# Optimization experiments

Hardware: AMD Instinct MI355X
Metric: run time of the kernel (lower is better)

Reference implementation:

```python
import jax, jax.numpy as jnp
import numpy as np

B, DIN, HID, DOUT, E, TOPK = 8192, 1024, 2048, 1024, 8, 2
GHID = HID // 2  # gating hidden


def setup_inputs() -> dict:
    key = jax.random.key(0)
    ks = jax.random.split(key, 16)
    s = lambda fan_in: 1.0 / np.sqrt(fan_in)
    return {
        "x": jax.random.normal(ks[0], (B, DIN), dtype=jnp.float32),
        # stacked expert params, leading axis = expert
        "w1": jax.random.uniform(ks[1], (E, DIN, HID), jnp.float32, -s(DIN), s(DIN)),
        "b1": jax.random.uniform(ks[2], (E, HID), jnp.float32, -s(DIN), s(DIN)),
        "w2": jax.random.uniform(ks[3], (E, HID, HID), jnp.float32, -s(HID), s(HID)),
        "b2": jax.random.uniform(ks[4], (E, HID), jnp.float32, -s(HID), s(HID)),
        "w3": jax.random.uniform(ks[5], (E, HID, DOUT), jnp.float32, -s(HID), s(HID)),
        "b3": jax.random.uniform(ks[6], (E, DOUT), jnp.float32, -s(HID), s(HID)),
        "wp": jax.random.uniform(ks[7], (E, DIN, HID), jnp.float32, -s(DIN), s(DIN)),
        "bp": jax.random.uniform(ks[8], (E, HID), jnp.float32, -s(DIN), s(DIN)),
        # gating network: Linear(DIN, GHID) -> ReLU -> Linear(GHID, E)
        "gw1": jax.random.uniform(ks[9], (DIN, GHID), jnp.float32, -s(DIN), s(DIN)),
        "gb1": jax.random.uniform(ks[10], (GHID,), jnp.float32, -s(DIN), s(DIN)),
        "gw2": jax.random.uniform(ks[11], (GHID, E), jnp.float32, -s(GHID), s(GHID)),
        "gb2": jax.random.uniform(ks[12], (E,), jnp.float32, -s(GHID), s(GHID)),
    }


def reference(x, w1, b1, w2, b2, w3, b3, wp, bp, gw1, gb1, gw2, gb2):
    # gating: [B, E]
    gate_logits = jnp.maximum(x @ gw1 + gb1, 0.0) @ gw2 + gb2
    topk_w, topk_i = jax.lax.top_k(gate_logits, TOPK)  # [B, K]
    topk_w = jax.nn.softmax(topk_w, axis=1)
    # dense per-expert residual MLP (dropout is identity in eval mode)
    h = jnp.maximum(jnp.einsum('bi,eih->beh', x, w1) + b1, 0.0)  # [B,E,HID]
    out = jnp.einsum('beh,ehg->beg', h, w2) + b2                  # [B,E,HID]
    identity = jnp.einsum('bi,eih->beh', x, wp) + bp              # projection
    out = jnp.maximum(out + identity, 0.0)
    expert_out = jnp.einsum('beh,eho->beo', out, w3) + b3         # [B,E,DOUT]
    # scatter top-k weights into dense [B, E] gate
    gate = jnp.zeros_like(gate_logits).at[jnp.arange(x.shape[0])[:, None], topk_i].set(topk_w)
    return jnp.einsum('beo,be->bo', expert_out, gate)             # [B, DOUT]
```

## Files before the change

### kernel.cpp

```cpp
#include <hip/hip_runtime.h>
#include <hip/hip_bf16.h>
#include <cstdint>
#include <cstddef>

#define TOK  8192
#define DIN  1024
#define HID  2048
#define DOUTN 1024
#define NEXP 8
#define GHID 1024

typedef __attribute__((ext_vector_type(8))) short bf16x8;
typedef __attribute__((ext_vector_type(4))) float floatx4;

__device__ __forceinline__ unsigned short f2b(float f) {
  unsigned int u = __float_as_uint(f);
  u += 0x7fffu + ((u >> 16) & 1u);
  return (unsigned short)(u >> 16);
}

__device__ __forceinline__ float b2f(unsigned short b) {
  return __uint_as_float(((unsigned int)b) << 16);
}

__device__ __forceinline__ void async_cp16(const unsigned short* g, char* lds) {
  __builtin_amdgcn_global_load_lds(
      (const __attribute__((address_space(1))) unsigned int*)g,
      (__attribute__((address_space(3))) unsigned int*)lds, 16, 0, 0);
}


__global__ void cvt_x_kernel(const float* __restrict__ src,
                             unsigned short* __restrict__ xb,
                             unsigned short* __restrict__ xcat, int n4) {
  int i = blockIdx.x * blockDim.x + threadIdx.x;
  if (i >= n4) return;
  float4 v = ((const float4*)src)[i];
  ushort4 hi, lo;
  hi.x = f2b(v.x); lo.x = f2b(v.x - b2f(hi.x));
  hi.y = f2b(v.y); lo.y = f2b(v.y - b2f(hi.y));
  hi.z = f2b(v.z); lo.z = f2b(v.z - b2f(hi.z));
  hi.w = f2b(v.w); lo.w = f2b(v.w - b2f(hi.w));
  ((ushort4*)xb)[i] = hi;
  int t = i >> 8;
  int kk = i & 255;
  ushort4* rowc = (ushort4*)(xcat + (size_t)t * 3072);
  rowc[kk] = hi;
  rowc[256 + kk] = hi;
  rowc[512 + kk] = lo;
}

__global__ void cvt_transpose_kernel(const float* __restrict__ src,
                                     unsigned short* __restrict__ dst,
                                     int K, int N) {
  __shared__ float tile[32][33];
  long e = blockIdx.z;
  src += e * (long)K * N;
  dst += e * (long)K * N;
  int n0 = blockIdx.x * 32, k0 = blockIdx.y * 32;
  int x = threadIdx.x, y = threadIdx.y;
#pragma unroll
  for (int i = 0; i < 4; i++)
    tile[y + 8 * i][x] = src[(long)(k0 + y + 8 * i) * N + n0 + x];
  __syncthreads();
#pragma unroll
  for (int i = 0; i < 4; i++)
    dst[(long)(n0 + y + 8 * i) * K + k0 + x] = f2b(tile[x][y + 8 * i]);
}

__global__ void cvt_gw1_kernel(const float* __restrict__ src,
                               unsigned short* __restrict__ dst) {
  __shared__ float tile[32][33];
  int n0 = blockIdx.x * 32, k0 = blockIdx.y * 32;
  int x = threadIdx.x, y = threadIdx.y;
#pragma unroll
  for (int i = 0; i < 4; i++)
    tile[y + 8 * i][x] = src[(long)(k0 + y + 8 * i) * GHID + n0 + x];
  __syncthreads();
#pragma unroll
  for (int i = 0; i < 4; i++) {
    float v = tile[x][y + 8 * i];
    unsigned short hi = f2b(v);
    unsigned short lo = f2b(v - b2f(hi));
    size_t r = (size_t)(n0 + y + 8 * i) * 3072 + k0 + x;
    dst[r] = hi;
    dst[r + 1024] = lo;
    dst[r + 2048] = hi;
  }
}


#define KLOOP(pa0, pa1, pb0, pb1, NKT)                                        \
  for (int kt = 0; kt < (NKT); ++kt) {                                        \
    __syncthreads();                                                          \
    async_cp16((pa0) + kt * 32, ldsA0);                                       \
    async_cp16((pa1) + kt * 32, ldsA0 + 4096);                                \
    async_cp16((pb0) + kt * 32, ldsB0);                                       \
    async_cp16((pb1) + kt * 32, ldsB0 + 4096);                                \
    __syncthreads();                                                          \
    bf16x8 af[4], bfr[4];                                                     \
    _Pragma("unroll") for (int i = 0; i < 4; i++) {                           \
      af[i] = *(const bf16x8*)(AsB + i * 1024);                               \
      bfr[i] = *(const bf16x8*)(BsB + i * 1024);                              \
    }                                                                         \
    _Pragma("unroll") for (int mi = 0; mi < 4; mi++)                          \
      _Pragma("unroll") for (int ni = 0; ni < 4; ni++)                        \
        acc[mi][ni] = __builtin_amdgcn_mfma_f32_16x16x32_bf16(                \
            af[mi], bfr[ni], acc[mi][ni], 0, 0, 0);                           \
  }

#define TILE_SETUP()                                                          \
  int tid = threadIdx.x;                                                      \
  int sr = tid >> 2;                                                          \
  int lchunk = (tid & 3) ^ ((sr >> 1) & 3);                                   \
  int koffA = lchunk * 8;                                                     \
  char* ldsA0 = (char*)As + (tid & 192) * 16;                                 \
  char* ldsB0 = (char*)Bs + (tid & 192) * 16;                                 \
  int lane = tid & 63, wv = tid >> 6;                                         \
  int wm = (wv >> 1) << 6, wn = (wv & 1) << 6;                                \
  int q = lane >> 4, l15 = lane & 15;                                         \
  int abase = l15 * 64 + ((q ^ ((l15 >> 1) & 3)) << 4);                       \
  const char* AsB = (const char*)As + wm * 64 + abase;                        \
  const char* BsB = (const char*)Bs + wn * 64 + abase;                        \
  floatx4 acc[4][4] = {};


__global__ __launch_bounds__(256, 2) void gating_mfma(
    const unsigned short* __restrict__ xcat,
    const unsigned short* __restrict__ gw1t3,
    const float* __restrict__ gb1, float* __restrict__ H) {
  __shared__ __align__(16) unsigned short As[128 * 32];
  __shared__ __align__(16) unsigned short Bs[128 * 32];
  TILE_SETUP();
  int row0 = blockIdx.y << 7, tn = blockIdx.x << 7;

  const unsigned short* a0p = xcat + (size_t)(row0 + sr) * 3072 + koffA;
  const unsigned short* a1p = xcat + (size_t)(row0 + 64 + sr) * 3072 + koffA;
  const unsigned short* b0p = gw1t3 + (size_t)(tn + sr) * 3072 + koffA;
  const unsigned short* b1p = gw1t3 + (size_t)(tn + 64 + sr) * 3072 + koffA;

  KLOOP(a0p, a1p, b0p, b1p, 3072 / 32);

  int crow = row0 + wm + q * 4;
  int ccol0 = tn + wn + l15;
#pragma unroll
  for (int ni = 0; ni < 4; ++ni) {
    int col = ccol0 + ni * 16;
    float bias = gb1[col];
#pragma unroll
    for (int mi = 0; mi < 4; ++mi)
#pragma unroll
      for (int rg = 0; rg < 4; ++rg) {
        int rr = crow + mi * 16 + rg;
        H[(size_t)rr * GHID + col] = fmaxf(acc[mi][ni][rg] + bias, 0.f);
      }
  }
}


__global__ void gating2_topk(const float* __restrict__ H,
                             const float* __restrict__ gw2,
                             const float* __restrict__ gb2,
                             int* __restrict__ gidx, float* __restrict__ gwt) {
  int wv = threadIdx.x >> 6, lane = threadIdx.x & 63;
  int t = blockIdx.x * 4 + wv;
  const float* hrow = H + (size_t)t * GHID;
  float acc[8] = {};
  for (int k = lane; k < GHID; k += 64) {
    float v = hrow[k];
    float4 g0 = *(const float4*)(gw2 + (size_t)k * 8);
    float4 g1 = *(const float4*)(gw2 + (size_t)k * 8 + 4);
    acc[0] += v * g0.x; acc[1] += v * g0.y; acc[2] += v * g0.z; acc[3] += v * g0.w;
    acc[4] += v * g1.x; acc[5] += v * g1.y; acc[6] += v * g1.z; acc[7] += v * g1.w;
  }
#pragma unroll
  for (int off = 32; off > 0; off >>= 1)
#pragma unroll
    for (int e = 0; e < 8; e++) acc[e] += __shfl_xor(acc[e], off);

  if (lane == 0) {
    float l[8];
#pragma unroll
    for (int e = 0; e < 8; e++) l[e] = acc[e] + gb2[e];
    int b0 = 0; float v0 = l[0];
#pragma unroll
    for (int e = 1; e < 8; e++) if (l[e] > v0) { v0 = l[e]; b0 = e; }
    int b1 = -1; float v1 = -3.4e38f;
#pragma unroll
    for (int e = 0; e < 8; e++)
      if (e != b0 && l[e] > v1) { v1 = l[e]; b1 = e; }
    float ex = expf(v1 - v0);
    float inv = 1.f / (1.f + ex);
    gidx[2 * t] = b0; gidx[2 * t + 1] = b1;
    gwt[2 * t] = inv; gwt[2 * t + 1] = ex * inv;
  }
}


__global__ void route_count(const int* __restrict__ gidx, int* cnt) {
  int t = blockIdx.x * blockDim.x + threadIdx.x;
  int lane = threadIdx.x & 63;
  int e0 = gidx[2 * t], e1 = gidx[2 * t + 1];
#pragma unroll 1
  for (int e = 0; e < NEXP; e++) {
    unsigned long long m0 = __ballot(e0 == e);
    if (m0 && lane == __ffsll(m0) - 1) atomicAdd(&cnt[e], (int)__popcll(m0));
    unsigned long long m1 = __ballot(e1 == e);
    if (m1 && lane == __ffsll(m1) - 1) atomicAdd(&cnt[e], (int)__popcll(m1));
  }
}

__global__ void route_scan(const int* __restrict__ cnt, int* base_, int* cur) {
  if (threadIdx.x == 0) {
    int s = 0;
    for (int e = 0; e < NEXP; e++) { base_[e] = s; cur[e] = s; s += cnt[e]; }
  }
}

__global__ void route_scatter(const int* __restrict__ gidx,
                              const float* __restrict__ gwt, int* cur,
                              int* __restrict__ rt, float* __restrict__ rw) {
  int t = blockIdx.x * blockDim.x + threadIdx.x;
  int lane = threadIdx.x & 63;
  int e0 = gidx[2 * t], e1 = gidx[2 * t + 1];
  float w0 = gwt[2 * t], w1 = gwt[2 * t + 1];
#pragma unroll 1
  for (int e = 0; e < NEXP; e++) {
#pragma unroll 1
    for (int s = 0; s < 2; s++) {
      int mye = s ? e1 : e0;
      unsigned long long m = __ballot(mye == e);
      if (m) {
        int leader = __ffsll(m) - 1;
        int bb = 0;
        if (lane == leader) bb = atomicAdd(&cur[e], (int)__popcll(m));
        bb = __shfl(bb, leader);
        if (mye == e) {
          int pos = bb + (int)__popcll(m & ((1ull << lane) - 1ull));
          rt[pos] = t;
          rw[pos] = s ? w1 : w0;
        }
      }
    }
  }
}


template <int MODE>
__global__ __launch_bounds__(256, 2) void moe_gemm(
    const unsigned short* __restrict__ xb, const unsigned short* __restrict__ hbuf,
    const unsigned short* __restrict__ obuf, const unsigned short* __restrict__ w1t,
    const unsigned short* __restrict__ wpt, const unsigned short* __restrict__ w2t,
    const unsigned short* __restrict__ w3t, const float* __restrict__ b1,
    const float* __restrict__ b2, const float* __restrict__ bp,
    const float* __restrict__ b3, const int* __restrict__ rt,
    const float* __restrict__ rw, const int* __restrict__ cnt,
    const int* __restrict__ base, unsigned short* __restrict__ hout,
    unsigned short* __restrict__ oout, float* __restrict__ dout) {
  __shared__ __align__(16) unsigned short As[128 * 32];
  __shared__ __align__(16) unsigned short Bs[128 * 32];

  int lt = blockIdx.y;
  int e = 0, cn = 0, ok = 0;
  for (e = 0; e < NEXP; ++e) {
    int c = cnt[e];
    int nt = (c + 127) >> 7;
    if (lt < nt) { cn = c; ok = 1; break; }
    lt -= nt;
  }
  if (!ok) return;
  int be = base[e];
  int row0 = lt << 7;
  int tn = blockIdx.x << 7;

  TILE_SETUP();

  int rl0 = row0 + sr, rl1 = row0 + 64 + sr;
  int cl0 = min(rl0, cn - 1), cl1 = min(rl1, cn - 1);

  if (MODE == 1) {
    const unsigned short* a0p = xb + (size_t)rt[be + cl0] * DIN + koffA;
    const unsigned short* a1p = xb + (size_t)rt[be + cl1] * DIN + koffA;
    const unsigned short* bw0 = w1t + ((size_t)e * HID + tn + sr) * DIN + koffA;
    const unsigned short* bw1 = w1t + ((size_t)e * HID + tn + 64 + sr) * DIN + koffA;
    KLOOP(a0p, a1p, bw0, bw1, DIN / 32);
  } else if (MODE == 2) {
    const unsigned short* a0p = hbuf + (size_t)(be + cl0) * HID + koffA;
    const unsigned short* a1p = hbuf + (size_t)(be + cl1) * HID + koffA;
    const unsigned short* bw0 = w2t + (size_t)e * HID * HID + (size_t)(tn + sr) * HID + koffA;
    const unsigned short* bw1 = w2t + (size_t)e * HID * HID + (size_t)(tn + 64 + sr) * HID + koffA;
    KLOOP(a0p, a1p, bw0, bw1, HID / 32);
    const unsigned short* a0q = xb + (size_t)rt[be + cl0] * DIN + koffA;
    const unsigned short* a1q = xb + (size_t)rt[be + cl1] * DIN + koffA;
    const unsigned short* bq0 = wpt + (size_t)e * HID * DIN + (size_t)(tn + sr) * DIN + koffA;
    const unsigned short* bq1 = wpt + (size_t)e * HID * DIN + (size_t)(tn + 64 + sr) * DIN + koffA;
    KLOOP(a0q, a1q, bq0, bq1, DIN / 32);
  } else {
    const unsigned short* a0p = obuf + (size_t)(be + cl0) * HID + koffA;
    const unsigned short* a1p = obuf + (size_t)(be + cl1) * HID + koffA;
    const unsigned short* bw0 = w3t + (size_t)e * DOUTN * HID + (size_t)(tn + sr) * HID + koffA;
    const unsigned short* bw1 = w3t + (size_t)e * DOUTN * HID + (size_t)(tn + 64 + sr) * HID + koffA;
    KLOOP(a0p, a1p, bw0, bw1, HID / 32);
  }

  int crow = row0 + wm + q * 4;
  int ccol0 = tn + wn + l15;
  if (MODE == 1) {
    const float* bb = b1 + (size_t)e * HID;
#pragma unroll
    for (int ni = 0; ni < 4; ++ni) {
      int col = ccol0 + ni * 16;
      float bias = bb[col];
#pragma unroll
      for (int mi = 0; mi < 4; ++mi)
#pragma unroll
        for (int rg = 0; rg < 4; ++rg) {
          int rr = crow + mi * 16 + rg;
          if (rr < cn) {
            float v = fmaxf(acc[mi][ni][rg] + bias, 0.f);
            hout[(size_t)(be + rr) * HID + col] = f2b(v);
          }
        }
    }
  } else if (MODE == 2) {
    const float* bb = b2 + (size_t)e * HID;
    const float* bq = bp + (size_t)e * HID;
#pragma unroll
    for (int ni = 0; ni < 4; ++ni) {
      int col = ccol0 + ni * 16;
      float bias = bb[col] + bq[col];
#pragma unroll
      for (int mi = 0; mi < 4; ++mi)
#pragma unroll
        for (int rg = 0; rg < 4; ++rg) {
          int rr = crow + mi * 16 + rg;
          if (rr < cn) {
            float v = fmaxf(acc[mi][ni][rg] + bias, 0.f);
            oout[(size_t)(be + rr) * HID + col] = f2b(v);
          }
        }
    }
  } else {
    const float* bb = b3 + (size_t)e * DOUTN;
    float biasv[4];
#pragma unroll
    for (int ni = 0; ni < 4; ++ni) biasv[ni] = bb[ccol0 + ni * 16];
#pragma unroll
    for (int mi = 0; mi < 4; ++mi)
#pragma unroll
      for (int rg = 0; rg < 4; ++rg) {
        int rr = crow + mi * 16 + rg;
        if (rr < cn) {
          int tk = rt[be + rr];
          float wgt = rw[be + rr];
#pragma unroll
          for (int ni = 0; ni < 4; ++ni) {
            int col = ccol0 + ni * 16;
            atomicAdd(dout + (size_t)tk * DOUTN + col,
                      (acc[mi][ni][rg] + biasv[ni]) * wgt);
          }
        }
      }
  }
}


extern "C" void kernel_launch(void* const* d_in, const int* in_sizes, int n_in,
                              void* d_out, int out_size, void* d_ws,
                              size_t ws_size, hipStream_t stream) {
  const float* x = (const float*)d_in[0];
  const float* w1 = (const float*)d_in[1];
  const float* b1 = (const float*)d_in[2];
  const float* w2 = (const float*)d_in[3];
  const float* b2 = (const float*)d_in[4];
  const float* w3 = (const float*)d_in[5];
  const float* b3 = (const float*)d_in[6];
  const float* wp = (const float*)d_in[7];
  const float* bp = (const float*)d_in[8];
  const float* gw1 = (const float*)d_in[9];
  const float* gb1 = (const float*)d_in[10];
  const float* gw2 = (const float*)d_in[11];
  const float* gb2 = (const float*)d_in[12];
  float* outp = (float*)d_out;
  char* ws = (char*)d_ws;

  const size_t o_w1t = 0;
  const size_t o_wpt = o_w1t + (size_t)NEXP * HID * DIN * 2;
  const size_t o_w2t = o_wpt + (size_t)NEXP * HID * DIN * 2;
  const size_t o_w3t = o_w2t + (size_t)NEXP * HID * HID * 2;
  const size_t o_xb  = o_w3t + (size_t)NEXP * DOUTN * HID * 2;
  const size_t o_hg  = o_xb + (size_t)TOK * DIN * 2;
  const size_t o_h   = o_hg + (size_t)TOK * GHID * 4;
  const size_t o_ob  = o_h + (size_t)2 * TOK * HID * 2;
  const size_t o_gidx = o_ob + (size_t)2 * TOK * HID * 2;
  const size_t o_gw  = o_gidx + (size_t)2 * TOK * 4;
  const size_t o_cnt = o_gw + (size_t)2 * TOK * 4;
  const size_t o_base = o_cnt + 128;
  const size_t o_cur = o_base + 128;
  const size_t o_rt  = o_cur + 128;
  const size_t o_rw  = o_rt + (size_t)2 * TOK * 4;
  const size_t o_xcat = o_ob;
  const size_t o_gw1t3 = o_h;

  unsigned short* w1t = (unsigned short*)(ws + o_w1t);
  unsigned short* wpt = (unsigned short*)(ws + o_wpt);
  unsigned short* w2t = (unsigned short*)(ws + o_w2t);
  unsigned short* w3t = (unsigned short*)(ws + o_w3t);
  unsigned short* xb = (unsigned short*)(ws + o_xb);
  float* hg = (float*)(ws + o_hg);
  unsigned short* hbuf = (unsigned short*)(ws + o_h);
  unsigned short* obuf = (unsigned short*)(ws + o_ob);
  unsigned short* xcat = (unsigned short*)(ws + o_xcat);
  unsigned short* gw1t3 = (unsigned short*)(ws + o_gw1t3);
  int* gidx = (int*)(ws + o_gidx);
  float* gwt = (float*)(ws + o_gw);
  int* cnt = (int*)(ws + o_cnt);
  int* basep = (int*)(ws + o_base);
  int* cur = (int*)(ws + o_cur);
  int* rtl = (int*)(ws + o_rt);
  float* rwl = (float*)(ws + o_rw);

  hipMemsetAsync(d_out, 0, (size_t)out_size * 4, stream);
  hipMemsetAsync(ws + o_cnt, 0, 32, stream);

  cvt_x_kernel<<<dim3(TOK * DIN / 4 / 256), 256, 0, stream>>>(x, xb, xcat, TOK * DIN / 4);
  cvt_gw1_kernel<<<dim3(GHID / 32, DIN / 32), dim3(32, 8), 0, stream>>>(gw1, gw1t3);
  cvt_transpose_kernel<<<dim3(HID / 32, DIN / 32, NEXP), dim3(32, 8), 0, stream>>>(w1, w1t, DIN, HID);
  cvt_transpose_kernel<<<dim3(HID / 32, DIN / 32, NEXP), dim3(32, 8), 0, stream>>>(wp, wpt, DIN, HID);
  cvt_transpose_kernel<<<dim3(HID / 32, HID / 32, NEXP), dim3(32, 8), 0, stream>>>(w2, w2t, HID, HID);
  cvt_transpose_kernel<<<dim3(DOUTN / 32, HID / 32, NEXP), dim3(32, 8), 0, stream>>>(w3, w3t, HID, DOUTN);

  gating_mfma<<<dim3(GHID / 128, TOK / 128), 256, 0, stream>>>(xcat, gw1t3, gb1, hg);
  gating2_topk<<<dim3(TOK / 4), 256, 0, stream>>>(hg, gw2, gb2, gidx, gwt);
  route_count<<<dim3(TOK / 256), 256, 0, stream>>>(gidx, cnt);
  route_scan<<<1, 64, 0, stream>>>(cnt, basep, cur);
  route_scatter<<<dim3(TOK / 256), 256, 0, stream>>>(gidx, gwt, cur, rtl, rwl);

  moe_gemm<1><<<dim3(HID / 128, 135), 256, 0, stream>>>(
      xb, hbuf, obuf, w1t, wpt, w2t, w3t, b1, b2, bp, b3, rtl, rwl, cnt, basep,
      hbuf, obuf, outp);
  moe_gemm<2><<<dim3(HID / 128, 135), 256, 0, stream>>>(
      xb, hbuf, obuf, w1t, wpt, w2t, w3t, b1, b2, bp, b3, rtl, rwl, cnt, basep,
      hbuf, obuf, outp);
  moe_gemm<3><<<dim3(DOUTN / 128, 135), 256, 0, stream>>>(
      xb, hbuf, obuf, w1t, wpt, w2t, w3t, b1, b2, bp, b3, rtl, rwl, cnt, basep,
      hbuf, obuf, outp);
}
```

Baseline: 1.123 ms.

## Concatenate h and gathered x into one K=3072 operand, replace atomics with combine

Rows are pre-gathered into a contiguous hx buffer ([h | x] per routed slot), and w2 and wp are packed into one [HID, 3072] weight, so MODE 2 runs a single K-loop instead of two with indirect x loads. The final GEMM writes weighted per-slot outputs to a scratch buffer, and a combine kernel sums each token's two slots, replacing atomicAdd and the output memset. Weight transposes use a wider 64x64 tile with vectorized stores, and launch bounds rise to 4 blocks per SM. The cost is extra gather and combine kernels plus more workspace, and the higher occupancy target may cause register spills.

Result: no change. 1.118 ms (-0.5%).

```diff
diff --git a/kernel.cpp b/kernel.cpp
--- a/kernel.cpp
+++ b/kernel.cpp
@@ -12,6 +12,7 @@
 
 typedef __attribute__((ext_vector_type(8))) short bf16x8;
 typedef __attribute__((ext_vector_type(4))) float floatx4;
+typedef __attribute__((ext_vector_type(8))) unsigned short ushort8v;
 
 __device__ __forceinline__ unsigned short f2b(float f) {
   unsigned int u = __float_as_uint(f);
@@ -50,22 +51,35 @@
   rowc[512 + kk] = lo;
 }
 
-__global__ void cvt_transpose_kernel(const float* __restrict__ src,
-                                     unsigned short* __restrict__ dst,
-                                     int K, int N) {
-  __shared__ float tile[32][33];
+__global__ void cvt_transpose_v2(const float* __restrict__ src,
+                                 unsigned short* __restrict__ dst, int N,
+                                 long sEstride, long dEstride, int ldDst) {
+  __shared__ __align__(16) unsigned short t[64][72];
   long e = blockIdx.z;
-  src += e * (long)K * N;
-  dst += e * (long)K * N;
-  int n0 = blockIdx.x * 32, k0 = blockIdx.y * 32;
-  int x = threadIdx.x, y = threadIdx.y;
-#pragma unroll
-  for (int i = 0; i < 4; i++)
-    tile[y + 8 * i][x] = src[(long)(k0 + y + 8 * i) * N + n0 + x];
+  src += e * sEstride;
+  dst += e * dEstride;
+  int n0 = blockIdx.x * 64, k0 = blockIdx.y * 64;
+  int tid = threadIdx.x;
+  int kr = tid >> 2, qc = tid & 3;
+  const float* s = src + (long)(k0 + kr) * N + n0 + qc * 16;
+#pragma unroll
+  for (int i = 0; i < 4; i++) {
+    float4 v = *(const float4*)(s + i * 4);
+    int nn = qc * 16 + i * 4;
+    t[nn + 0][kr] = f2b(v.x);
+    t[nn + 1][kr] = f2b(v.y);
+    t[nn + 2][kr] = f2b(v.z);
+    t[nn + 3][kr] = f2b(v.w);
+  }
   __syncthreads();
-#pragma unroll
-  for (int i = 0; i < 4; i++)
-    dst[(long)(n0 + y + 8 * i) * K + k0 + x] = f2b(tile[x][y + 8 * i]);
+  int c = tid & 7;
+  int nr = tid >> 3;
+#pragma unroll
+  for (int p = 0; p < 2; p++) {
+    int n = nr + 32 * p;
+    ushort8v v = *(const ushort8v*)&t[n][c * 8];
+    *(ushort8v*)(dst + (long)(n0 + n) * ldDst + k0 + c * 8) = v;
+  }
 }
 
 __global__ void cvt_gw1_kernel(const float* __restrict__ src,
@@ -125,7 +139,7 @@
   floatx4 acc[4][4] = {};
 
 
-__global__ __launch_bounds__(256, 2) void gating_mfma(
+__global__ __launch_bounds__(256, 4) void gating_mfma(
     const unsigned short* __restrict__ xcat,
     const unsigned short* __restrict__ gw1t3,
     const float* __restrict__ gb1, float* __restrict__ H) {
@@ -219,7 +233,8 @@
 
 __global__ void route_scatter(const int* __restrict__ gidx,
                               const float* __restrict__ gwt, int* cur,
-                              int* __restrict__ rt, float* __restrict__ rw) {
+                              int* __restrict__ rt, float* __restrict__ rw,
+                              int* __restrict__ inv) {
   int t = blockIdx.x * blockDim.x + threadIdx.x;
   int lane = threadIdx.x & 63;
   int e0 = gidx[2 * t], e1 = gidx[2 * t + 1];
@@ -239,24 +254,46 @@
           int pos = bb + (int)__popcll(m & ((1ull << lane) - 1ull));
           rt[pos] = t;
           rw[pos] = s ? w1 : w0;
+          inv[2 * t + s] = pos;
         }
       }
     }
   }
 }
 
+__global__ void xgather_kernel(const unsigned short* __restrict__ xb,
+                               const int* __restrict__ rt,
+                               unsigned short* __restrict__ hx) {
+  int slot = blockIdx.x;
+  int c = threadIdx.x;
+  int t = rt[slot];
+  ((ushort8v*)(hx + (size_t)slot * 3072 + 2048))[c] =
+      ((const ushort8v*)(xb + (size_t)t * 1024))[c];
+}
+
+__global__ void combine_kernel(const float* __restrict__ s3,
+                               const int* __restrict__ inv,
+                               float* __restrict__ out) {
+  int t = blockIdx.x;
+  int c = threadIdx.x;
+  const float4* r0 = (const float4*)(s3 + (size_t)inv[2 * t] * DOUTN);
+  const float4* r1 = (const float4*)(s3 + (size_t)inv[2 * t + 1] * DOUTN);
+  float4 a = r0[c], b = r1[c];
+  float4 o = {a.x + b.x, a.y + b.y, a.z + b.z, a.w + b.w};
+  ((float4*)(out + (size_t)t * DOUTN))[c] = o;
+}
+
 
 template <int MODE>
-__global__ __launch_bounds__(256, 2) void moe_gemm(
-    const unsigned short* __restrict__ xb, const unsigned short* __restrict__ hbuf,
-    const unsigned short* __restrict__ obuf, const unsigned short* __restrict__ w1t,
-    const unsigned short* __restrict__ wpt, const unsigned short* __restrict__ w2t,
+__global__ __launch_bounds__(256, 4) void moe_gemm(
+    const unsigned short* __restrict__ hx, const unsigned short* __restrict__ obuf,
+    const unsigned short* __restrict__ w1t, const unsigned short* __restrict__ w2p,
     const unsigned short* __restrict__ w3t, const float* __restrict__ b1,
     const float* __restrict__ b2, const float* __restrict__ bp,
-    const float* __restrict__ b3, const int* __restrict__ rt,
-    const float* __restrict__ rw, const int* __restrict__ cnt,
-    const int* __restrict__ base, unsigned short* __restrict__ hout,
-    unsigned short* __restrict__ oout, float* __restrict__ dout) {
+    const float* __restrict__ b3, const float* __restrict__ rw,
+    const int* __restrict__ cnt, const int* __restrict__ base,
+    unsigned short* __restrict__ hxout, unsigned short* __restrict__ oout,
+    float* __restrict__ s3) {
   __shared__ __align__(16) unsigned short As[128 * 32];
   __shared__ __align__(16) unsigned short Bs[128 * 32];
 
@@ -279,27 +316,22 @@
   int cl0 = min(rl0, cn - 1), cl1 = min(rl1, cn - 1);
 
   if (MODE == 1) {
-    const unsigned short* a0p = xb + (size_t)rt[be + cl0] * DIN + koffA;
-    const unsigned short* a1p = xb + (size_t)rt[be + cl1] * DIN + koffA;
+    const unsigned short* a0p = hx + (size_t)(be + cl0) * 3072 + 2048 + koffA;
+    const unsigned short* a1p = hx + (size_t)(be + cl1) * 3072 + 2048 + koffA;
     const unsigned short* bw0 = w1t + ((size_t)e * HID + tn + sr) * DIN + koffA;
     const unsigned short* bw1 = w1t + ((size_t)e * HID + tn + 64 + sr) * DIN + koffA;
     KLOOP(a0p, a1p, bw0, bw1, DIN / 32);
   } else if (MODE == 2) {
-    const unsigned short* a0p = hbuf + (size_t)(be + cl0) * HID + koffA;
-    const unsigned short* a1p = hbuf + (size_t)(be + cl1) * HID + koffA;
-    const unsigned short* bw0 = w2t + (size_t)e * HID * HID + (size_t)(tn + sr) * HID + koffA;
-    const unsigned short* bw1 = w2t + (size_t)e * HID * HID + (size_t)(tn + 64 + sr) * HID + koffA;
-    KLOOP(a0p, a1p, bw0, bw1, HID / 32);
-    const unsigned short* a0q = xb + (size_t)rt[be + cl0] * DIN + koffA;
-    const unsigned short* a1q = xb + (size_t)rt[be + cl1] * DIN + koffA;
-    const unsigned short* bq0 = wpt + (size_t)e * HID * DIN + (size_t)(tn + sr) * DIN + koffA;
-    const unsigned short* bq1 = wpt + (size_t)e * HID * DIN + (size_t)(tn + 64 + sr) * DIN + koffA;
-    KLOOP(a0q, a1q, bq0, bq1, DIN / 32);
+    const unsigned short* a0p = hx + (size_t)(be + cl0) * 3072 + koffA;
+    const unsigned short* a1p = hx + (size_t)(be + cl1) * 3072 + koffA;
+    const unsigned short* bw0 = w2p + ((size_t)e * HID + tn + sr) * 3072 + koffA;
+    const unsigned short* bw1 = w2p + ((size_t)e * HID + tn + 64 + sr) * 3072 + koffA;
+    KLOOP(a0p, a1p, bw0, bw1, 3072 / 32);
   } else {
     const unsigned short* a0p = obuf + (size_t)(be + cl0) * HID + koffA;
     const unsigned short* a1p = obuf + (size_t)(be + cl1) * HID + koffA;
-    const unsigned short* bw0 = w3t + (size_t)e * DOUTN * HID + (size_t)(tn + sr) * HID + koffA;
-    const unsigned short* bw1 = w3t + (size_t)e * DOUTN * HID + (size_t)(tn + 64 + sr) * HID + koffA;
+    const unsigned short* bw0 = w3t + ((size_t)e * DOUTN + tn + sr) * HID + koffA;
+    const unsigned short* bw1 = w3t + ((size_t)e * DOUTN + tn + 64 + sr) * HID + koffA;
     KLOOP(a0p, a1p, bw0, bw1, HID / 32);
   }
 
@@ -318,7 +350,7 @@
           int rr = crow + mi * 16 + rg;
           if (rr < cn) {
             float v = fmaxf(acc[mi][ni][rg] + bias, 0.f);
-            hout[(size_t)(be + rr) * HID + col] = f2b(v);
+            hxout[(size_t)(be + rr) * 3072 + col] = f2b(v);
           }
         }
     }
@@ -351,13 +383,12 @@
       for (int rg = 0; rg < 4; ++rg) {
         int rr = crow + mi * 16 + rg;
         if (rr < cn) {
-          int tk = rt[be + rr];
           float wgt = rw[be + rr];
 #pragma unroll
           for (int ni = 0; ni < 4; ++ni) {
             int col = ccol0 + ni * 16;
-            atomicAdd(dout + (size_t)tk * DOUTN + col,
-                      (acc[mi][ni][rg] + biasv[ni]) * wgt);
+            s3[(size_t)(be + rr) * DOUTN + col] =
+                (acc[mi][ni][rg] + biasv[ni]) * wgt;
           }
         }
       }
@@ -384,34 +415,35 @@
   float* outp = (float*)d_out;
   char* ws = (char*)d_ws;
 
-  const size_t o_w1t = 0;
-  const size_t o_wpt = o_w1t + (size_t)NEXP * HID * DIN * 2;
-  const size_t o_w2t = o_wpt + (size_t)NEXP * HID * DIN * 2;
-  const size_t o_w3t = o_w2t + (size_t)NEXP * HID * HID * 2;
+  const size_t o_w2p = 0;
+  const size_t o_w3t = o_w2p + (size_t)NEXP * HID * 3072 * 2;
   const size_t o_xb  = o_w3t + (size_t)NEXP * DOUTN * HID * 2;
-  const size_t o_hg  = o_xb + (size_t)TOK * DIN * 2;
-  const size_t o_h   = o_hg + (size_t)TOK * GHID * 4;
-  const size_t o_ob  = o_h + (size_t)2 * TOK * HID * 2;
-  const size_t o_gidx = o_ob + (size_t)2 * TOK * HID * 2;
+  const size_t o_w1t = o_xb + (size_t)TOK * DIN * 2;
+  const size_t o_hg  = o_w1t + (size_t)NEXP * HID * DIN * 2;
+  const size_t o_hx  = o_hg + (size_t)TOK * GHID * 4;
+  const size_t o_gw1t3 = o_hx + (size_t)2 * TOK * 3072 * 2;
+  const size_t o_gidx = o_gw1t3 + (size_t)GHID * 3072 * 2;
   const size_t o_gw  = o_gidx + (size_t)2 * TOK * 4;
   const size_t o_cnt = o_gw + (size_t)2 * TOK * 4;
   const size_t o_base = o_cnt + 128;
   const size_t o_cur = o_base + 128;
   const size_t o_rt  = o_cur + 128;
   const size_t o_rw  = o_rt + (size_t)2 * TOK * 4;
-  const size_t o_xcat = o_ob;
-  const size_t o_gw1t3 = o_h;
-
-  unsigned short* w1t = (unsigned short*)(ws + o_w1t);
-  unsigned short* wpt = (unsigned short*)(ws + o_wpt);
-  unsigned short* w2t = (unsigned short*)(ws + o_w2t);
+  const size_t o_inv = o_rw + (size_t)2 * TOK * 4;
+  const size_t o_xcat = o_hx;
+  const size_t o_ob   = o_w1t;
+  const size_t o_s3   = o_w2p;
+
+  unsigned short* w2p = (unsigned short*)(ws + o_w2p);
   unsigned short* w3t = (unsigned short*)(ws + o_w3t);
   unsigned short* xb = (unsigned short*)(ws + o_xb);
+  unsigned short* w1t = (unsigned short*)(ws + o_w1t);
   float* hg = (float*)(ws + o_hg);
-  unsigned short* hbuf = (unsigned short*)(ws + o_h);
+  unsigned short* hx = (unsigned short*)(ws + o_hx);
+  unsigned short* gw1t3 = (unsigned short*)(ws + o_gw1t3);
+  unsigned short* xcat = (unsigned short*)(ws + o_xcat);
   unsigned short* obuf = (unsigned short*)(ws + o_ob);
-  unsigned short* xcat = (unsigned short*)(ws + o_xcat);
-  unsigned short* gw1t3 = (unsigned short*)(ws + o_gw1t3);
+  float* s3 = (float*)(ws + o_s3);
   int* gidx = (int*)(ws + o_gidx);
   float* gwt = (float*)(ws + o_gw);
   int* cnt = (int*)(ws + o_cnt);
@@ -419,30 +451,34 @@
   int* cur = (int*)(ws + o_cur);
   int* rtl = (int*)(ws + o_rt);
   float* rwl = (float*)(ws + o_rw);
-
-  hipMemsetAsync(d_out, 0, (size_t)out_size * 4, stream);
+  int* invp = (int*)(ws + o_inv);
+
   hipMemsetAsync(ws + o_cnt, 0, 32, stream);
 
   cvt_x_kernel<<<dim3(TOK * DIN / 4 / 256), 256, 0, stream>>>(x, xb, xcat, TOK * DIN / 4);
   cvt_gw1_kernel<<<dim3(GHID / 32, DIN / 32), dim3(32, 8), 0, stream>>>(gw1, gw1t3);
-  cvt_transpose_kernel<<<dim3(HID / 32, DIN / 32, NEXP), dim3(32, 8), 0, stream>>>(w1, w1t, DIN, HID);
-  cvt_transpose_kernel<<<dim3(HID / 32, DIN / 32, NEXP), dim3(32, 8), 0, stream>>>(wp, wpt, DIN, HID);
-  cvt_transpose_kernel<<<dim3(HID / 32, HID / 32, NEXP), dim3(32, 8), 0, stream>>>(w2, w2t, HID, HID);
-  cvt_transpose_kernel<<<dim3(DOUTN / 32, HID / 32, NEXP), dim3(32, 8), 0, stream>>>(w3, w3t, HID, DOUTN);
+  cvt_transpose_v2<<<dim3(HID / 64, DIN / 64, NEXP), 256, 0, stream>>>(
+      w1, w1t, HID, (long)DIN * HID, (long)HID * DIN, DIN);
+  cvt_transpose_v2<<<dim3(HID / 64, HID / 64, NEXP), 256, 0, stream>>>(
+      w2, w2p, HID, (long)HID * HID, (long)HID * 3072, 3072);
+  cvt_transpose_v2<<<dim3(HID / 64, DIN / 64, NEXP), 256, 0, stream>>>(
+      wp, w2p + 2048, HID, (long)DIN * HID, (long)HID * 3072, 3072);
+  cvt_transpose_v2<<<dim3(DOUTN / 64, HID / 64, NEXP), 256, 0, stream>>>(
+      w3, w3t, DOUTN, (long)HID * DOUTN, (long)DOUTN * HID, HID);
 
   gating_mfma<<<dim3(GHID / 128, TOK / 128), 256, 0, stream>>>(xcat, gw1t3, gb1, hg);
   gating2_topk<<<dim3(TOK / 4), 256, 0, stream>>>(hg, gw2, gb2, gidx, gwt);
   route_count<<<dim3(TOK / 256), 256, 0, stream>>>(gidx, cnt);
   route_scan<<<1, 64, 0, stream>>>(cnt, basep, cur);
-  route_scatter<<<dim3(TOK / 256), 256, 0, stream>>>(gidx, gwt, cur, rtl, rwl);
+  route_scatter<<<dim3(TOK / 256), 256, 0, stream>>>(gidx, gwt, cur, rtl, rwl, invp);
+  xgather_kernel<<<dim3(2 * TOK), 128, 0, stream>>>(xb, rtl, hx);
 
   moe_gemm<1><<<dim3(HID / 128, 135), 256, 0, stream>>>(
-      xb, hbuf, obuf, w1t, wpt, w2t, w3t, b1, b2, bp, b3, rtl, rwl, cnt, basep,
-      hbuf, obuf, outp);
+      hx, obuf, w1t, w2p, w3t, b1, b2, bp, b3, rwl, cnt, basep, hx, obuf, s3);
   moe_gemm<2><<<dim3(HID / 128, 135), 256, 0, stream>>>(
-      xb, hbuf, obuf, w1t, wpt, w2t, w3t, b1, b2, bp, b3, rtl, rwl, cnt, basep,
-      hbuf, obuf, outp);
+      hx, obuf, w1t, w2p, w3t, b1, b2, bp, b3, rwl, cnt, basep, hx, obuf, s3);
   moe_gemm<3><<<dim3(DOUTN / 128, 135), 256, 0, stream>>>(
-      xb, hbuf, obuf, w1t, wpt, w2t, w3t, b1, b2, bp, b3, rtl, rwl, cnt, basep,
-      hbuf, obuf, outp);
-}
+      hx, obuf, w1t, w2p, w3t, b1, b2, bp, b3, rwl, cnt, basep, hx, obuf, s3);
+
+  combine_kernel<<<dim3(TOK), 256, 0, stream>>>(s3, invp, outp);
+}
```
